# Kernel optimization log

Hardware: AMD Instinct MI355X
Metric: run time of the kernel (lower is better)

## Reference

```python
import jax, jax.numpy as jnp
import numpy as np

B, N, DIM = 2, 128, 128
H, DH = 8, 32
DI = H * DH          # dim_inner = 256
DM = 2 * DI          # mlp_expansion_factor * dim_inner = 512
MAXDEG = 2
S = 1 + MAXDEG + MAXDEG  # 5
M1, M2 = 3, 5        # 2l+1 for degrees 1,2


def setup_inputs() -> dict:
    key = jax.random.key(0)
    ks = jax.random.split(key, 24)
    rn = lambda k, shp, sc=1.0: jax.random.normal(k, shp, jnp.float32) * sc
    s_d = DIM ** -0.5
    s_m = DM ** -0.5
    s_i = DI ** -0.5
    return {
        "h":    rn(ks[0], (B, N, DIM)),
        "t_ij": rn(ks[1], (B, N, N, DIM)),
        "r1":   rn(ks[2], (B, N, N, M1)),
        "r2":   rn(ks[3], (B, N, N, M2)),
        "x1":   rn(ks[4], (B, N, DIM, M1)),
        "x2":   rn(ks[5], (B, N, DIM, M2)),
        # LayerNorm gains (bias=False)
        "g_hi": jnp.ones((DIM,), jnp.float32),
        "g_hj": jnp.ones((DIM,), jnp.float32),
        # projections (stored as [in, out])
        "Wq":  rn(ks[6],  (DIM, DI), s_d),
        "Wk":  rn(ks[7],  (DIM, DI), s_d),
        "Wv1": rn(ks[8],  (DIM, DM), s_d), "bv1": jnp.zeros((DM,), jnp.float32),
        "Wv2": rn(ks[9],  (DM, S * DI), s_m), "bv2": jnp.zeros((S * DI,), jnp.float32),
        "Wpv1": rn(ks[10], (DIM, DM), s_d), "bpv1": jnp.zeros((DM,), jnp.float32),
        "Wpv2": rn(ks[11], (DM, S * DI), s_m), "bpv2": jnp.zeros((S * DI,), jnp.float32),
        "Wek": rn(ks[12], (DIM, S * DI), s_d),
        "Wev": rn(ks[13], (DIM, S * DI), s_d),
        "Wg":  rn(ks[14], (DIM, H * S), s_d), "bg": jnp.zeros((H * S,), jnp.float32),
        "Wo":  rn(ks[15], (DI, DIM), s_i),
    }


def _ln(x, g):
    mu = x.mean(-1, keepdims=True)
    var = ((x - mu) ** 2).mean(-1, keepdims=True)
    return (x - mu) / jnp.sqrt(var + 1e-5) * g


def reference(h, t_ij, r1, r2, x1, x2, g_hi, g_hj, Wq, Wk, Wv1, bv1, Wv2, bv2,
              Wpv1, bpv1, Wpv2, bpv2, Wek, Wev, Wg, bg, Wo):
    silu = jax.nn.silu
    hi = _ln(h, g_hi)  # b n d
    hj = _ln(h, g_hj)
    # queries/keys: b h n dh
    q = (hi @ Wq).reshape(B, N, H, DH).transpose(0, 2, 1, 3)
    k = (hj @ Wk).reshape(B, N, H, DH).transpose(0, 2, 1, 3)
    # node values / post-attn values: b h n s dh
    v  = (silu(hj @ Wv1 + bv1) @ Wv2 + bv2).reshape(B, N, S, H, DH).transpose(0, 3, 1, 2, 4)
    pv = (silu(hj @ Wpv1 + bpv1) @ Wpv2 + bpv2).reshape(B, N, S, H, DH).transpose(0, 3, 1, 2, 4)
    # edge keys/values: b h i j s dh
    ek = silu(t_ij @ Wek).reshape(B, N, N, S, H, DH).transpose(0, 4, 1, 2, 3, 5)
    ev = (t_ij @ Wev).reshape(B, N, N, S, H, DH).transpose(0, 4, 1, 2, 3, 5)
    # keys elementwise-conditioned by edge keys, then score over dh
    sim = jnp.einsum('bhid,bhjd,bhijsd->bhijs', q, k, ek)
    attn = jax.nn.softmax(sim, axis=3)  # softmax over j (dim=-2 of b h i j s)
    # sea_ij: b h i j s dh
    sea = attn[..., None] * v[:, :, None] + ev * pv[:, :, None]
    # gates: b h i 1 s 1
    gates = jax.nn.sigmoid(hi @ Wg + bg).reshape(B, N, H, S).transpose(0, 2, 1, 3)
    out = sea * gates[:, :, :, None, :, None]
    # merge heads -> b i j s (h dh), combine -> b i j s dim
    out = out.transpose(0, 2, 3, 4, 1, 5).reshape(B, N, N, S, DI) @ Wo
    # split along s: (1, maxdeg, maxdeg) = (h_scales, r_scales, x_scales)
    h_out = h + out[..., 0, :].sum(axis=2)  # sum over j
    x1_out = (jnp.einsum('bjdm,bijd->bidm', x1, out[..., 3, :])
              + jnp.einsum('bijm,bijd->bidm', r1, out[..., 1, :]))
    x2_out = (jnp.einsum('bjdm,bijd->bidm', x2, out[..., 4, :])
              + jnp.einsum('bijm,bijd->bidm', r2, out[..., 2, :]))
    return (h_out, x1_out, x2_out)
```

## Files before the change

### kernel.cpp

```cpp
#include <hip/hip_runtime.h>
#include <math.h>

#define BB 2
#define NN 128
#define DD 128
#define DI 256
#define DM 512
#define SS 5
#define SDI 1280
#define HS 40
#define M1 3
#define M2 5

typedef __attribute__((ext_vector_type(8))) short bf16x8_t;
typedef __attribute__((ext_vector_type(4))) float f32x4_t;
typedef __attribute__((ext_vector_type(4))) float f32x4v;

#define MFMA __builtin_amdgcn_mfma_f32_16x16x32_bf16

__device__ __forceinline__ float sigm(float x){ return __fdividef(1.0f, 1.0f + __expf(-x)); }
__device__ __forceinline__ unsigned short f2bf(float f){
    union { float f; unsigned u; } v; v.f = f;
    unsigned r = v.u + 0x7FFFu + ((v.u>>16)&1u);
    return (unsigned short)(r>>16);
}
__device__ __forceinline__ unsigned pk2(float a, float b){
    return (unsigned)f2bf(a) | ((unsigned)f2bf(b)<<16);
}
__device__ __forceinline__ float bflo(unsigned u){ union{unsigned u; float f;} v; v.u = u<<16; return v.f; }
__device__ __forceinline__ float bfhi(unsigned u){ union{unsigned u; float f;} v; v.u = u & 0xFFFF0000u; return v.f; }

__global__ __launch_bounds__(256) void prep(
    const float* __restrict__ h,
    const float* __restrict__ g_hi, const float* __restrict__ g_hj,
    const float* __restrict__ Wq, const float* __restrict__ Wk,
    const float* __restrict__ Wv1, const float* __restrict__ Wpv1,
    const float* __restrict__ Wg,
    const float* __restrict__ Wek, const float* __restrict__ Wev,
    const float* __restrict__ Wo, const float* __restrict__ Wv2,
    const float* __restrict__ Wpv2,
    const float* __restrict__ x1, const float* __restrict__ x2,
    unsigned short* __restrict__ hi_ws, unsigned short* __restrict__ hj_ws,
    unsigned short* __restrict__ WekT, unsigned short* __restrict__ WevT,
    unsigned short* __restrict__ WoT, unsigned short* __restrict__ W2T,
    unsigned short* __restrict__ WnT,
    float* __restrict__ x1T, float* __restrict__ x2T)
{
    const int bx = blockIdx.x, tid = threadIdx.x;
    __shared__ unsigned short sLT[64*65];
    if (bx < 408){
        const float* src; unsigned short* dst; int W, ldD, R0, C0;
        int t = bx;
        if (t < 160){ src=Wv2;  dst=W2T;            W=SDI; ldD=DM;  R0=(t%20)*64; C0=(t/20)*64; }
        else if (t < 320){ t-=160; src=Wpv2; dst=W2T + SDI*DM; W=SDI; ldD=DM; R0=(t%20)*64; C0=(t/20)*64; }
        else if (t < 360){ t-=320; src=Wek; dst=WekT; W=SDI; ldD=DD; R0=(t%20)*64; C0=(t/20)*64; }
        else if (t < 400){ t-=360; src=Wev; dst=WevT; W=SDI; ldD=DD; R0=(t%20)*64; C0=(t/20)*64; }
        else { t-=400; src=Wo; dst=WoT; W=DD; ldD=DI; R0=(t%2)*64; C0=(t/2)*64; }
        const int tx = tid & 63, ty = tid >> 6;
        #pragma unroll
        for (int k=0;k<16;++k){
            int c = C0 + 4*k + ty;
            sLT[tx*65 + 4*k + ty] = f2bf(src[(size_t)c*W + R0 + tx]);
        }
        __syncthreads();
        #pragma unroll
        for (int k=0;k<16;++k){
            int rr = 4*k + ty;
            dst[(size_t)(R0+rr)*ldD + C0 + tx] = sLT[rr*65 + tx];
        }
    } else if (bx < 664){
        const int node = bx - 408;
        if (tid < 64){
            float h0 = h[node*DD + tid], h1 = h[node*DD + 64 + tid];
            float s1 = h0 + h1, s2 = h0*h0 + h1*h1;
            #pragma unroll
            for (int off=32; off; off>>=1){ s1 += __shfl_xor(s1,off); s2 += __shfl_xor(s2,off); }
            float mu   = s1*(1.0f/DD);
            float var  = s2*(1.0f/DD) - mu*mu;
            float rstd = rsqrtf(var + 1e-5f);
            float c0 = (h0-mu)*rstd, c1 = (h1-mu)*rstd;
            hi_ws[node*DD + tid]      = f2bf(c0*g_hi[tid]);
            hi_ws[node*DD + 64 + tid] = f2bf(c1*g_hi[64+tid]);
            hj_ws[node*DD + tid]      = f2bf(c0*g_hj[tid]);
            hj_ws[node*DD + 64 + tid] = f2bf(c1*g_hj[64+tid]);
        }
        for (int f = node*256 + tid; f < 1584*DD; f += 256*256){
            int row = f >> 7, d = f & 127;
            float v;
            if (row < 256)       v = Wq[d*DI + row];
            else if (row < 304){ int c = row-256; v = (c < HS) ? Wg[d*HS + c] : 0.0f; }
            else if (row < 560)  v = Wk[d*DI + (row-304)];
            else if (row < 1072) v = Wv1[d*DM + (row-560)];
            else                 v = Wpv1[d*DM + (row-1072)];
            WnT[f] = f2bf(v);
        }
    } else {
        const int t = bx - 664;
        const int bb = t >> 7, j = t & 127;
        const int d = tid & 127, half = tid >> 7;
        if (half == 0){
            #pragma unroll
            for (int m=0;m<M1;++m)
                x1T[((size_t)(bb*M1+m)*NN + j)*DD + d] =
                    x1[(((size_t)bb*NN + j)*DD + d)*M1 + m];
        } else {
            #pragma unroll
            for (int m=0;m<M2;++m)
                x2T[((size_t)(bb*M2+m)*NN + j)*DD + d] =
                    x2[(((size_t)bb*NN + j)*DD + d)*M2 + m];
        }
    }
}

__global__ __launch_bounds__(256,4) void node_gemm(
    const unsigned short* __restrict__ WnT,
    const unsigned short* __restrict__ hi_ws, const unsigned short* __restrict__ hj_ws,
    const float* __restrict__ bg, const float* __restrict__ bv1, const float* __restrict__ bpv1,
    float* __restrict__ q_ws, float* __restrict__ k_ws,
    float* __restrict__ g_ws, unsigned short* __restrict__ hid_ws)
{
    const int bx = blockIdx.x;
    const int tile = bx % 99, nq = bx / 99;
    const int tid = threadIdx.x, lane = tid&63, w = tid>>6;
    const int l15 = lane&15, g4 = lane>>4;
    const int ntile = nq*4 + w;
    const unsigned short* A  = WnT + (size_t)(tile*16 + l15)*DD + 8*g4;
    const unsigned short* Bp = ((tile < 19) ? hi_ws : hj_ws) + (size_t)(ntile*16 + l15)*DD + 8*g4;
    f32x4_t c = {0.f,0.f,0.f,0.f};
    #pragma unroll
    for (int ks=0; ks<4; ++ks)
        c = MFMA(*(const bf16x8_t*)(A + 32*ks), *(const bf16x8_t*)(Bp + 32*ks), c, 0,0,0);
    const int node = ntile*16 + l15;
    const int col0 = tile*16 + 4*g4;
    if (tile < 16){
        f32x4_t* dst = (f32x4_t*)(q_ws + (size_t)node*DI + col0);
        *dst = c;
    } else if (tile < 19){
        #pragma unroll
        for (int r=0;r<4;++r){
            int cc = col0 + r - 256;
            if (cc < HS) g_ws[node*HS + cc] = sigm(c[r] + bg[cc]);
        }
    } else if (tile < 35){
        f32x4_t* dst = (f32x4_t*)(k_ws + (size_t)node*DI + (col0-304));
        *dst = c;
    } else if (tile < 67){
        int cc = col0 - 560;
        float s0 = c[0]+bv1[cc], s1 = c[1]+bv1[cc+1], s2 = c[2]+bv1[cc+2], s3 = c[3]+bv1[cc+3];
        s0 *= sigm(s0); s1 *= sigm(s1); s2 *= sigm(s2); s3 *= sigm(s3);
        uint2 pkk; pkk.x = pk2(s0,s1); pkk.y = pk2(s2,s3);
        *(uint2*)(hid_ws + (size_t)node*1024 + cc) = pkk;
    } else {
        int cc = col0 - 1072;
        float s0 = c[0]+bpv1[cc], s1 = c[1]+bpv1[cc+1], s2 = c[2]+bpv1[cc+2], s3 = c[3]+bpv1[cc+3];
        s0 *= sigm(s0); s1 *= sigm(s1); s2 *= sigm(s2); s3 *= sigm(s3);
        uint2 pkk; pkk.x = pk2(s0,s1); pkk.y = pk2(s2,s3);
        *(uint2*)(hid_ws + (size_t)node*1024 + 512 + cc) = pkk;
    }
}

__global__ __launch_bounds__(256,4) void v2_gemm(
    const unsigned short* __restrict__ W2T,
    const unsigned short* __restrict__ hid_ws,
    const float* __restrict__ bv2, const float* __restrict__ bpv2,
    unsigned short* __restrict__ vpv_ws)
{
    const int bx = blockIdx.x;
    const int otile = bx % 160, nq = bx / 160;
    const int tid = threadIdx.x, lane = tid&63, w = tid>>6;
    const int l15 = lane&15, g4 = lane>>4;
    const int ntile = nq*4 + w;
    const int obase = otile*16;
    const int koff = (obase < SDI) ? 0 : 512;
    const unsigned short* A  = W2T + (size_t)(obase + l15)*DM + 8*g4;
    const unsigned short* Bp = hid_ws + (size_t)(ntile*16 + l15)*1024 + koff + 8*g4;
    f32x4_t c = {0.f,0.f,0.f,0.f};
    #pragma unroll
    for (int ks=0; ks<16; ++ks)
        c = MFMA(*(const bf16x8_t*)(A + 32*ks), *(const bf16x8_t*)(Bp + 32*ks), c, 0,0,0);
    const int node = ntile*16 + l15;
    const int o0 = obase + 4*g4;
    const float* bias = (obase < SDI) ? bv2 : bpv2;
    const int ob = (obase < SDI) ? o0 : (o0 - SDI);
    float v0 = c[0]+bias[ob], v1 = c[1]+bias[ob+1], v2 = c[2]+bias[ob+2], v3 = c[3]+bias[ob+3];
    uint2 pkk; pkk.x = pk2(v0,v1); pkk.y = pk2(v2,v3);
    *(uint2*)(vpv_ws + (size_t)node*2560 + o0) = pkk;
}

#define SH_T   0
#define SH_QK  16384
#define SH_SIM 49152
#define SH_Q   59392

__global__ __launch_bounds__(512,4) void simh(
    const float* __restrict__ t_ij,
    const unsigned short* __restrict__ WekT,
    const float* __restrict__ q_ws, const float* __restrict__ k_ws,
    float* __restrict__ sim_ws)
{
    __shared__ __align__(16) char sm[60416];
    float* sSIM = (float*)(sm + SH_SIM);
    float* sQf  = (float*)(sm + SH_Q);

    const int bx0 = blockIdx.x;
    const int bx = ((bx0 & 7) << 6) | (bx0 >> 3);
    const int node = bx >> 1, jh = bx & 1;
    const int b = node >> 7;
    const int j0 = jh*64;
    const int tid = threadIdx.x, lane = tid&63, w = tid>>6;
    const int l15 = lane&15, g4 = lane>>4;

    if (tid < DI) sQf[tid] = q_ws[(size_t)node*DI + tid];
    {
        const int j = tid>>3, seg = tid&7;
        const float* src = t_ij + (size_t)(node*NN + j0 + j)*DD + seg*16;
        char* row = sm + SH_T + j*256;
        const int swz = (j&7)<<4;
        #pragma unroll
        for (int u=0;u<4;++u){
            f32x4v tv = __builtin_nontemporal_load((const f32x4v*)(src + 4*u));
            uint2 pkk; pkk.x = pk2(tv[0],tv[1]); pkk.y = pk2(tv[2],tv[3]);
            *(uint2*)(row + ((2*(seg*16+4*u)) ^ swz)) = pkk;
        }
    }
    __syncthreads();
    {
        const int j = tid>>3, seg = tid&7;
        const float* kr = k_ws + (size_t)(b*NN + j0 + j)*DI + seg*32;
        char* row = sm + SH_QK + j*512;
        const int swz = (j&7)<<4;
        #pragma unroll
        for (int u=0;u<8;++u){
            float4 kv = *(const float4*)(kr + 4*u);
            const float* qv = sQf + seg*32 + 4*u;
            uint2 pkk; pkk.x = pk2(kv.x*qv[0], kv.y*qv[1]); pkk.y = pk2(kv.z*qv[2], kv.w*qv[3]);
            *(uint2*)(row + ((2*(seg*32+4*u)) ^ swz)) = pkk;
        }
    }
    bf16x8_t bT[4][4];
    #pragma unroll
    for (int jt=0;jt<4;++jt){
        const int jc = jt*16 + l15;
        const char* row = sm + SH_T + jc*256;
        const int swz = (jc&7)<<4;
        #pragma unroll
        for (int ks=0;ks<4;++ks)
            bT[jt][ks] = *(const bf16x8_t*)(row + ((2*(32*ks+8*g4)) ^ swz));
    }
    __syncthreads();

    for (int p5=0; p5<5; ++p5){
        const int p = w + 8*p5;
        const unsigned short* ap = WekT + (size_t)(2*p)*16*DD + (size_t)l15*DD + 8*g4;
        bf16x8_t a0[4], a1[4];
        #pragma unroll
        for (int ks=0;ks<4;++ks){
            a0[ks] = *(const bf16x8_t*)(ap + 32*ks);
            a1[ks] = *(const bf16x8_t*)(ap + 16*DD + 32*ks);
        }
        const int hs = w*SS + p5;
        const int o0 = 32*p + 4*g4;
        const int qk0 = o0 & 255;
        #pragma unroll
        for (int jt=0;jt<4;++jt){
            f32x4_t c0 = {0.f,0.f,0.f,0.f}, c1 = {0.f,0.f,0.f,0.f};
            #pragma unroll
            for (int ks=0;ks<4;++ks){
                c0 = MFMA(a0[ks], bT[jt][ks], c0, 0,0,0);
                c1 = MFMA(a1[ks], bT[jt][ks], c1, 0,0,0);
            }
            const int jr = jt*16 + l15;
            const char* qrow = sm + SH_QK + jr*512;
            const int swz = (jr&7)<<4;
            uint2 u0 = *(const uint2*)(qrow + ((2*qk0) ^ swz));
            uint2 u1 = *(const uint2*)(qrow + ((2*(qk0+16)) ^ swz));
            float part =
                (c0[0]*sigm(c0[0]))*bflo(u0.x) + (c0[1]*sigm(c0[1]))*bfhi(u0.x)
              + (c0[2]*sigm(c0[2]))*bflo(u0.y) + (c0[3]*sigm(c0[3]))*bfhi(u0.y)
              + (c1[0]*sigm(c1[0]))*bflo(u1.x) + (c1[1]*sigm(c1[1]))*bfhi(u1.x)
              + (c1[2]*sigm(c1[2]))*bflo(u1.y) + (c1[3]*sigm(c1[3]))*bfhi(u1.y);
            part += __shfl_xor(part, 16);
            part += __shfl_xor(part, 32);
            if (g4 == 0) sSIM[jr*HS + hs] = part;
        }
    }
    __syncthreads();
    {
        float* dst = sim_ws + (size_t)node*NN*HS + j0*HS;
        for (int t2=tid; t2<64*HS; t2+=512) dst[t2] = sSIM[t2];
    }
}

__global__ __launch_bounds__(256) void softmax_k(
    float* __restrict__ sim_ws, const float* __restrict__ g_ws)
{
    const int node = blockIdx.x;
    const int tid = threadIdx.x, lane = tid&63, w = tid>>6;
    float* srow = sim_ws + (size_t)node*NN*HS;
    #pragma unroll
    for (int u=0; u<10; ++u){
        const int hs = w*10 + u;
        const float gt = g_ws[node*HS + hs];
        float v0 = srow[lane*HS + hs];
        float v1 = srow[(lane+64)*HS + hs];
        float m = fmaxf(v0,v1);
        #pragma unroll
        for (int off=32; off; off>>=1) m = fmaxf(m, __shfl_xor(m,off));
        float e0 = __expf(v0-m), e1 = __expf(v1-m);
        float ssum = e0+e1;
        #pragma unroll
        for (int off=32; off; off>>=1) ssum += __shfl_xor(ssum,off);
        float inv = __fdividef(gt, ssum);
        srow[lane*HS + hs]      = e0*inv;
        srow[(lane+64)*HS + hs] = e1*inv;
    }
}

#define OH_T   0
#define OH_P   16384
#define OH_AT  49152
#define OH_G   59392
#define OH_W1  59552
#define OH_W2  60320

__global__ __launch_bounds__(512,4) void outh(
    const float* __restrict__ t_ij,
    const unsigned short* __restrict__ WevT, const unsigned short* __restrict__ WoT,
    const unsigned short* __restrict__ vpv_ws,
    const float* __restrict__ attn_ws,
    const float* __restrict__ g_ws,
    const float* __restrict__ r1, const float* __restrict__ r2,
    const float* __restrict__ x1T, const float* __restrict__ x2T,
    float* __restrict__ p_out)
{
    __shared__ __align__(16) char sm[61600];
    float* sATT = (float*)(sm + OH_AT);
    float* sG   = (float*)(sm + OH_G);
    float* sW1  = (float*)(sm + OH_W1);
    float* sW2  = (float*)(sm + OH_W2);

    const int bx0 = blockIdx.x;
    const int bx = ((bx0 & 7) << 6) | (bx0 >> 3);
    const int node = bx >> 1, jh = bx & 1;
    const int b = node >> 7;
    const int j0 = jh*64;
    const int tid = threadIdx.x, lane = tid&63, w = tid>>6;
    const int l15 = lane&15, g4 = lane>>4;

    {
        const int j = tid>>3, seg = tid&7;
        const float* src = t_ij + (size_t)(node*NN + j0 + j)*DD + seg*16;
        char* row = sm + OH_T + j*256;
        const int swz = (j&7)<<4;
        #pragma unroll
        for (int u=0;u<4;++u){
            f32x4v tv = __builtin_nontemporal_load((const f32x4v*)(src + 4*u));
            uint2 pkk; pkk.x = pk2(tv[0],tv[1]); pkk.y = pk2(tv[2],tv[3]);
            *(uint2*)(row + ((2*(seg*16+4*u)) ^ swz)) = pkk;
        }
    }
    {
        const float* asrc = attn_ws + (size_t)node*NN*HS + j0*HS;
        for (int t2=tid; t2<64*HS; t2+=512) sATT[t2] = asrc[t2];
    }
    if (tid < HS) sG[tid] = g_ws[node*HS + tid];
    if (tid < 64*M1) sW1[tid] = r1[((size_t)node*NN + j0)*M1 + tid];
    if (tid < 64*M2) sW2[tid] = r2[((size_t)node*NN + j0)*M2 + tid];
    bf16x8_t bWo[8];
    {
        const unsigned short* wr = WoT + (size_t)(w*16 + l15)*DI + 8*g4;
        #pragma unroll
        for (int ks=0;ks<8;++ks) bWo[ks] = *(const bf16x8_t*)(wr + 32*ks);
    }
    __syncthreads();

    const int d = w*16 + l15;
    float ah = 0.f;
    float ax1[M1] = {0.f,0.f,0.f};
    float ax2[M2] = {0.f,0.f,0.f,0.f,0.f};

    #pragma unroll
    for (int s=0; s<SS; ++s){
        #pragma unroll
        for (int mloc=0; mloc<2; ++mloc){
            const int mt = w*2 + mloc;
            const unsigned short* ap = WevT + (size_t)(s*DI + mt*16 + l15)*DD + 8*g4;
            bf16x8_t aa[4];
            #pragma unroll
            for (int ks=0;ks<4;++ks) aa[ks] = *(const bf16x8_t*)(ap + 32*ks);
            const int m0 = mt*16 + 4*g4;
            const int hh = mt >> 1;
            const float gtv = sG[hh*SS + s];
            #pragma unroll
            for (int jt=0;jt<4;++jt){
                const int jc = jt*16 + l15;
                bf16x8_t bT[4];
                {
                    const char* row = sm + OH_T + jc*256;
                    const int swz = (jc&7)<<4;
                    #pragma unroll
                    for (int ks=0;ks<4;++ks)
                        bT[ks] = *(const bf16x8_t*)(row + ((2*(32*ks+8*g4)) ^ swz));
                }
                f32x4_t c = {0.f,0.f,0.f,0.f};
                #pragma unroll
                for (int ks=0;ks<4;++ks) c = MFMA(aa[ks], bT[ks], c, 0,0,0);
                const float atv = sATT[jc*HS + hh*SS + s];
                const unsigned short* vb = vpv_ws + (size_t)(b*NN + j0 + jc)*2560 + s*DI + m0;
                uint2 vv = *(const uint2*)vb;
                uint2 pp = *(const uint2*)(vb + SDI);
                float q0 = atv*bflo(vv.x) + gtv*c[0]*bflo(pp.x);
                float q1 = atv*bfhi(vv.x) + gtv*c[1]*bfhi(pp.x);
                float q2 = atv*bflo(vv.y) + gtv*c[2]*bflo(pp.y);
                float q3 = atv*bfhi(vv.y) + gtv*c[3]*bfhi(pp.y);
                uint2 pkk; pkk.x = pk2(q0,q1); pkk.y = pk2(q2,q3);
                *(uint2*)(sm + OH_P + jc*512 + ((2*m0) ^ ((jc&7)<<4))) = pkk;
            }
        }
        __syncthreads();
        #pragma unroll
        for (int jt=0; jt<4; ++jt){
            const int arow = jt*16 + l15;
            const char* pb = sm + OH_P + arow*512;
            const int aswz = (arow&7)<<4;
            f32x4_t c = {0.f,0.f,0.f,0.f};
            #pragma unroll
            for (int ks=0;ks<8;++ks){
                bf16x8_t a = *(const bf16x8_t*)(pb + ((64*ks + 16*g4) ^ aswz));
                c = MFMA(a, bWo[ks], c, 0,0,0);
            }
            if (s == 0){
                ah += c[0]+c[1]+c[2]+c[3];
            } else if (s == 1){
                #pragma unroll
                for (int r=0;r<4;++r){
                    const int jr = jt*16 + 4*g4 + r;
                    #pragma unroll
                    for (int m=0;m<M1;++m) ax1[m] = fmaf(sW1[jr*M1+m], c[r], ax1[m]);
                }
            } else if (s == 2){
                #pragma unroll
                for (int r=0;r<4;++r){
                    const int jr = jt*16 + 4*g4 + r;
                    #pragma unroll
                    for (int m=0;m<M2;++m) ax2[m] = fmaf(sW2[jr*M2+m], c[r], ax2[m]);
                }
            } else if (s == 3){
                #pragma unroll
                for (int r=0;r<4;++r){
                    const int jr = j0 + jt*16 + 4*g4 + r;
                    #pragma unroll
                    for (int m=0;m<M1;++m)
                        ax1[m] = fmaf(x1T[((size_t)(b*M1+m)*NN + jr)*DD + d], c[r], ax1[m]);
                }
            } else {
                #pragma unroll
                for (int r=0;r<4;++r){
                    const int jr = j0 + jt*16 + 4*g4 + r;
                    #pragma unroll
                    for (int m=0;m<M2;++m)
                        ax2[m] = fmaf(x2T[((size_t)(b*M2+m)*NN + jr)*DD + d], c[r], ax2[m]);
                }
            }
        }
        __syncthreads();
    }

    {
        float v0 = ah;
        float v1 = ax1[0], v2 = ax1[1], v3 = ax1[2];
        float v4 = ax2[0], v5 = ax2[1], v6 = ax2[2], v7 = ax2[3], v8 = ax2[4];
        v0 += __shfl_xor(v0,16); v0 += __shfl_xor(v0,32);
        v1 += __shfl_xor(v1,16); v1 += __shfl_xor(v1,32);
        v2 += __shfl_xor(v2,16); v2 += __shfl_xor(v2,32);
        v3 += __shfl_xor(v3,16); v3 += __shfl_xor(v3,32);
        v4 += __shfl_xor(v4,16); v4 += __shfl_xor(v4,32);
        v5 += __shfl_xor(v5,16); v5 += __shfl_xor(v5,32);
        v6 += __shfl_xor(v6,16); v6 += __shfl_xor(v6,32);
        v7 += __shfl_xor(v7,16); v7 += __shfl_xor(v7,32);
        v8 += __shfl_xor(v8,16); v8 += __shfl_xor(v8,32);
        if (g4 == 0){
            float* pb = p_out + (size_t)bx*9*DD + d;
            pb[0*DD] = v0;
            pb[1*DD] = v1; pb[2*DD] = v2; pb[3*DD] = v3;
            pb[4*DD] = v4; pb[5*DD] = v5; pb[6*DD] = v6; pb[7*DD] = v7; pb[8*DD] = v8;
        }
    }
}

__global__ __launch_bounds__(128) void combine(
    const float* __restrict__ h, const float* __restrict__ p_out,
    float* __restrict__ out_h, float* __restrict__ out_x1, float* __restrict__ out_x2)
{
    const int node = blockIdx.x, d = threadIdx.x;
    const float* pa = p_out + (size_t)(node*2+0)*9*DD + d;
    const float* pb = p_out + (size_t)(node*2+1)*9*DD + d;
    out_h[(size_t)node*DD + d] = h[(size_t)node*DD + d] + pa[0] + pb[0];
    #pragma unroll
    for (int m=0;m<M1;++m)
        out_x1[((size_t)node*DD + d)*M1 + m] = pa[(1+m)*DD] + pb[(1+m)*DD];
    #pragma unroll
    for (int m=0;m<M2;++m)
        out_x2[((size_t)node*DD + d)*M2 + m] = pa[(4+m)*DD] + pb[(4+m)*DD];
}

extern "C" void kernel_launch(void* const* d_in, const int* in_sizes, int n_in,
                              void* d_out, int out_size, void* d_ws, size_t ws_size,
                              hipStream_t stream)
{
    (void)in_sizes; (void)n_in; (void)out_size; (void)ws_size;
    const float* h    = (const float*)d_in[0];
    const float* t_ij = (const float*)d_in[1];
    const float* r1   = (const float*)d_in[2];
    const float* r2   = (const float*)d_in[3];
    const float* x1   = (const float*)d_in[4];
    const float* x2   = (const float*)d_in[5];
    const float* g_hi = (const float*)d_in[6];
    const float* g_hj = (const float*)d_in[7];
    const float* Wq   = (const float*)d_in[8];
    const float* Wk   = (const float*)d_in[9];
    const float* Wv1  = (const float*)d_in[10];
    const float* bv1  = (const float*)d_in[11];
    const float* Wv2  = (const float*)d_in[12];
    const float* bv2  = (const float*)d_in[13];
    const float* Wpv1 = (const float*)d_in[14];
    const float* bpv1 = (const float*)d_in[15];
    const float* Wpv2 = (const float*)d_in[16];
    const float* bpv2 = (const float*)d_in[17];
    const float* Wek  = (const float*)d_in[18];
    const float* Wev  = (const float*)d_in[19];
    const float* Wg   = (const float*)d_in[20];
    const float* bg   = (const float*)d_in[21];
    const float* Wo   = (const float*)d_in[22];

    float* fb     = (float*)d_ws;
    float* q_ws   = fb;
    float* k_ws   = q_ws   + 65536;
    float* g_ws   = k_ws   + 65536;
    float* sim_ws = g_ws   + 10240;
    float* p_out  = sim_ws + 1310720;
    float* x1T    = p_out  + 589824;
    float* x2T    = x1T    + 98304;
    unsigned short* hi_ws  = (unsigned short*)(x2T + 163840);
    unsigned short* hj_ws  = hi_ws  + 32768;
    unsigned short* hid_ws = hj_ws  + 32768;
    unsigned short* vpv_ws = hid_ws + 262144;
    unsigned short* WekT   = vpv_ws + 655360;
    unsigned short* WevT   = WekT   + 163840;
    unsigned short* WoT    = WevT   + 163840;
    unsigned short* W2T    = WoT    + 32768;
    unsigned short* WnT    = W2T    + 1310720;

    float* out_h  = (float*)d_out;
    float* out_x1 = out_h  + BB*NN*DD;
    float* out_x2 = out_x1 + BB*NN*DD*M1;

    prep<<<920, 256, 0, stream>>>(h, g_hi, g_hj, Wq, Wk, Wv1, Wpv1, Wg,
        Wek, Wev, Wo, Wv2, Wpv2, x1, x2,
        hi_ws, hj_ws, WekT, WevT, WoT, W2T, WnT, x1T, x2T);

    node_gemm<<<396, 256, 0, stream>>>(WnT, hi_ws, hj_ws, bg, bv1, bpv1,
        q_ws, k_ws, g_ws, hid_ws);

    v2_gemm<<<640, 256, 0, stream>>>(W2T, hid_ws, bv2, bpv2, vpv_ws);

    simh<<<512, 512, 0, stream>>>(t_ij, WekT, q_ws, k_ws, sim_ws);

    softmax_k<<<256, 256, 0, stream>>>(sim_ws, g_ws);

    outh<<<512, 512, 0, stream>>>(t_ij, WevT, WoT, vpv_ws, sim_ws, g_ws,
        r1, r2, x1T, x2T, p_out);

    combine<<<256, 128, 0, stream>>>(h, p_out, out_h, out_x1, out_x2);
}
```

Baseline: 184.3 us.

## Reduce s=0..2 over j before the Wo projection and defer Wo to combine

For the scale channels whose j-weights do not depend on d (s=0,1,2), the outh kernel now sums the gated values over j in the DI space first, weighting by r1/r2. It writes these partial sums to a workspace, and the combine kernel applies the Wo projection to them afterwards. This drops three of the five per-tile Wo MFMA passes, along with their LDS staging and barriers. Only s=3 and s=4 still go through the P tile and Wo in outh, with the x loads issued ahead of the MFMAs. The cost is more cross-lane shuffle reductions, more register pressure for the accumulators, and a combine kernel that now does a small 9x256x128 matvec per node.

Result: faster. 172.5 us (-6.4%).

```diff
diff --git a/kernel.cpp b/kernel.cpp
--- a/kernel.cpp
+++ b/kernel.cpp
@@ -323,6 +323,80 @@
 #define OH_W1  59552
 #define OH_W2  60320
 
+#define EV_BODY(S, EPILOG)                                                        \
+    _Pragma("unroll")                                                             \
+    for (int mloc=0; mloc<2; ++mloc){                                             \
+        const int mt = w*2 + mloc;                                                \
+        const int m0 = mt*16 + 4*g4;                                              \
+        uint2 vvr[4], ppr[4];                                                     \
+        _Pragma("unroll")                                                         \
+        for (int jt=0;jt<4;++jt){                                                 \
+            const unsigned short* vb = vpv_ws + (size_t)(b*NN + j0 + jt*16 + l15)*2560 + (S)*DI + m0; \
+            vvr[jt] = *(const uint2*)vb;                                          \
+            ppr[jt] = *(const uint2*)(vb + SDI);                                  \
+        }                                                                         \
+        const unsigned short* ap = WevT + (size_t)((S)*DI + mt*16 + l15)*DD + 8*g4; \
+        bf16x8_t aa[4];                                                           \
+        _Pragma("unroll")                                                         \
+        for (int ks=0;ks<4;++ks) aa[ks] = *(const bf16x8_t*)(ap + 32*ks);         \
+        const int hh = mt >> 1;                                                   \
+        const float gtv = sG[hh*SS + (S)];                                        \
+        _Pragma("unroll")                                                         \
+        for (int jt=0;jt<4;++jt){                                                 \
+            const int jc = jt*16 + l15;                                           \
+            bf16x8_t bT[4];                                                       \
+            {   const char* row_ = sm + OH_T + jc*256;                            \
+                const int swz_ = (jc&7)<<4;                                       \
+                _Pragma("unroll")                                                 \
+                for (int ks=0;ks<4;++ks)                                          \
+                    bT[ks] = *(const bf16x8_t*)(row_ + ((2*(32*ks+8*g4)) ^ swz_)); } \
+            f32x4_t c = {0.f,0.f,0.f,0.f};                                        \
+            _Pragma("unroll")                                                     \
+            for (int ks=0;ks<4;++ks) c = MFMA(aa[ks], bT[ks], c, 0,0,0);          \
+            const float atv = sATT[jc*HS + hh*SS + (S)];                          \
+            float g_[4];                                                          \
+            g_[0] = atv*bflo(vvr[jt].x) + gtv*c[0]*bflo(ppr[jt].x);               \
+            g_[1] = atv*bfhi(vvr[jt].x) + gtv*c[1]*bfhi(ppr[jt].x);               \
+            g_[2] = atv*bflo(vvr[jt].y) + gtv*c[2]*bflo(ppr[jt].y);               \
+            g_[3] = atv*bfhi(vvr[jt].y) + gtv*c[3]*bfhi(ppr[jt].y);               \
+            EPILOG                                                                \
+        }                                                                         \
+    }
+
+#define WO_X(XT, MM, AX)                                                          \
+    _Pragma("unroll")                                                             \
+    for (int jt=0; jt<4; ++jt){                                                   \
+        float xv[4*(MM)];                                                         \
+        _Pragma("unroll")                                                         \
+        for (int r_=0;r_<4;++r_){                                                 \
+            const int jr = j0 + jt*16 + 4*g4 + r_;                                \
+            _Pragma("unroll")                                                     \
+            for (int m_=0;m_<(MM);++m_)                                           \
+                xv[r_*(MM)+m_] = XT[((size_t)(b*(MM)+m_)*NN + jr)*DD + d];        \
+        }                                                                         \
+        const int arow = jt*16 + l15;                                             \
+        const char* pbp = sm + OH_P + arow*512;                                   \
+        const int aswz = (arow&7)<<4;                                             \
+        f32x4_t c = {0.f,0.f,0.f,0.f};                                            \
+        _Pragma("unroll")                                                         \
+        for (int ks=0;ks<8;++ks){                                                 \
+            bf16x8_t a = *(const bf16x8_t*)(pbp + ((64*ks + 16*g4) ^ aswz));      \
+            c = MFMA(a, bWo[ks], c, 0,0,0);                                       \
+        }                                                                         \
+        _Pragma("unroll")                                                         \
+        for (int r_=0;r_<4;++r_){                                                 \
+            _Pragma("unroll")                                                     \
+            for (int m_=0;m_<(MM);++m_) AX[m_] = fmaf(xv[r_*(MM)+m_], c[r_], AX[m_]); \
+        }                                                                         \
+    }
+
+#define RED_WRITE(VAL, ROW, T_)                                                   \
+    { float v_ = (VAL);                                                           \
+      v_ += __shfl_xor(v_,1); v_ += __shfl_xor(v_,2);                             \
+      v_ += __shfl_xor(v_,4); v_ += __shfl_xor(v_,8);                             \
+      if (l15 == 0)                                                               \
+          pdst[(ROW)*256 + (w*2 + ((T_)>>2))*16 + 4*g4 + ((T_)&3)] = v_; }
+
 __global__ __launch_bounds__(512,4) void outh(
     const float* __restrict__ t_ij,
     const unsigned short* __restrict__ WevT, const unsigned short* __restrict__ WoT,
@@ -331,7 +405,7 @@
     const float* __restrict__ g_ws,
     const float* __restrict__ r1, const float* __restrict__ r2,
     const float* __restrict__ x1T, const float* __restrict__ x2T,
-    float* __restrict__ p_out)
+    float* __restrict__ p012, float* __restrict__ p34)
 {
     __shared__ __align__(16) char sm[61600];
     float* sATT = (float*)(sm + OH_AT);
@@ -366,110 +440,85 @@
     if (tid < HS) sG[tid] = g_ws[node*HS + tid];
     if (tid < 64*M1) sW1[tid] = r1[((size_t)node*NN + j0)*M1 + tid];
     if (tid < 64*M2) sW2[tid] = r2[((size_t)node*NN + j0)*M2 + tid];
+    __syncthreads();
+
+    float* pdst = p012 + (size_t)(jh*256 + node)*9*256;
+
+    {
+        float a0[8] = {0,0,0,0,0,0,0,0};
+        EV_BODY(0, {
+            _Pragma("unroll")
+            for (int k_=0;k_<4;++k_) a0[mloc*4+k_] += g_[k_];
+        })
+        #pragma unroll
+        for (int t_=0;t_<8;++t_) RED_WRITE(a0[t_], 0, t_)
+    }
+    {
+        float a1[M1][8];
+        #pragma unroll
+        for (int m_=0;m_<M1;++m_)
+            #pragma unroll
+            for (int t_=0;t_<8;++t_) a1[m_][t_] = 0.f;
+        EV_BODY(1, {
+            _Pragma("unroll")
+            for (int m_=0;m_<M1;++m_){
+                const float wgt = sW1[jc*M1 + m_];
+                _Pragma("unroll")
+                for (int k_=0;k_<4;++k_) a1[m_][mloc*4+k_] = fmaf(wgt, g_[k_], a1[m_][mloc*4+k_]);
+            }
+        })
+        #pragma unroll
+        for (int m_=0;m_<M1;++m_)
+            #pragma unroll
+            for (int t_=0;t_<8;++t_) RED_WRITE(a1[m_][t_], 1+m_, t_)
+    }
+    {
+        float a2[M2][8];
+        #pragma unroll
+        for (int m_=0;m_<M2;++m_)
+            #pragma unroll
+            for (int t_=0;t_<8;++t_) a2[m_][t_] = 0.f;
+        EV_BODY(2, {
+            _Pragma("unroll")
+            for (int m_=0;m_<M2;++m_){
+                const float wgt = sW2[jc*M2 + m_];
+                _Pragma("unroll")
+                for (int k_=0;k_<4;++k_) a2[m_][mloc*4+k_] = fmaf(wgt, g_[k_], a2[m_][mloc*4+k_]);
+            }
+        })
+        #pragma unroll
+        for (int m_=0;m_<M2;++m_)
+            #pragma unroll
+            for (int t_=0;t_<8;++t_) RED_WRITE(a2[m_][t_], 4+m_, t_)
+    }
+
+    const int d = w*16 + l15;
     bf16x8_t bWo[8];
     {
-        const unsigned short* wr = WoT + (size_t)(w*16 + l15)*DI + 8*g4;
+        const unsigned short* wr = WoT + (size_t)d*DI + 8*g4;
         #pragma unroll
         for (int ks=0;ks<8;++ks) bWo[ks] = *(const bf16x8_t*)(wr + 32*ks);
     }
-    __syncthreads();
-
-    const int d = w*16 + l15;
-    float ah = 0.f;
     float ax1[M1] = {0.f,0.f,0.f};
     float ax2[M2] = {0.f,0.f,0.f,0.f,0.f};
 
-    #pragma unroll
-    for (int s=0; s<SS; ++s){
-        #pragma unroll
-        for (int mloc=0; mloc<2; ++mloc){
-            const int mt = w*2 + mloc;
-            const unsigned short* ap = WevT + (size_t)(s*DI + mt*16 + l15)*DD + 8*g4;
-            bf16x8_t aa[4];
-            #pragma unroll
-            for (int ks=0;ks<4;++ks) aa[ks] = *(const bf16x8_t*)(ap + 32*ks);
-            const int m0 = mt*16 + 4*g4;
-            const int hh = mt >> 1;
-            const float gtv = sG[hh*SS + s];
-            #pragma unroll
-            for (int jt=0;jt<4;++jt){
-                const int jc = jt*16 + l15;
-                bf16x8_t bT[4];
-                {
-                    const char* row = sm + OH_T + jc*256;
-                    const int swz = (jc&7)<<4;
-                    #pragma unroll
-                    for (int ks=0;ks<4;++ks)
-                        bT[ks] = *(const bf16x8_t*)(row + ((2*(32*ks+8*g4)) ^ swz));
-                }
-                f32x4_t c = {0.f,0.f,0.f,0.f};
-                #pragma unroll
-                for (int ks=0;ks<4;++ks) c = MFMA(aa[ks], bT[ks], c, 0,0,0);
-                const float atv = sATT[jc*HS + hh*SS + s];
-                const unsigned short* vb = vpv_ws + (size_t)(b*NN + j0 + jc)*2560 + s*DI + m0;
-                uint2 vv = *(const uint2*)vb;
-                uint2 pp = *(const uint2*)(vb + SDI);
-                float q0 = atv*bflo(vv.x) + gtv*c[0]*bflo(pp.x);
-                float q1 = atv*bfhi(vv.x) + gtv*c[1]*bfhi(pp.x);
-                float q2 = atv*bflo(vv.y) + gtv*c[2]*bflo(pp.y);
-                float q3 = atv*bfhi(vv.y) + gtv*c[3]*bfhi(pp.y);
-                uint2 pkk; pkk.x = pk2(q0,q1); pkk.y = pk2(q2,q3);
-                *(uint2*)(sm + OH_P + jc*512 + ((2*m0) ^ ((jc&7)<<4))) = pkk;
-            }
-        }
-        __syncthreads();
-        #pragma unroll
-        for (int jt=0; jt<4; ++jt){
-            const int arow = jt*16 + l15;
-            const char* pb = sm + OH_P + arow*512;
-            const int aswz = (arow&7)<<4;
-            f32x4_t c = {0.f,0.f,0.f,0.f};
-            #pragma unroll
-            for (int ks=0;ks<8;++ks){
-                bf16x8_t a = *(const bf16x8_t*)(pb + ((64*ks + 16*g4) ^ aswz));
-                c = MFMA(a, bWo[ks], c, 0,0,0);
-            }
-            if (s == 0){
-                ah += c[0]+c[1]+c[2]+c[3];
-            } else if (s == 1){
-                #pragma unroll
-                for (int r=0;r<4;++r){
-                    const int jr = jt*16 + 4*g4 + r;
-                    #pragma unroll
-                    for (int m=0;m<M1;++m) ax1[m] = fmaf(sW1[jr*M1+m], c[r], ax1[m]);
-                }
-            } else if (s == 2){
-                #pragma unroll
-                for (int r=0;r<4;++r){
-                    const int jr = jt*16 + 4*g4 + r;
-                    #pragma unroll
-                    for (int m=0;m<M2;++m) ax2[m] = fmaf(sW2[jr*M2+m], c[r], ax2[m]);
-                }
-            } else if (s == 3){
-                #pragma unroll
-                for (int r=0;r<4;++r){
-                    const int jr = j0 + jt*16 + 4*g4 + r;
-                    #pragma unroll
-                    for (int m=0;m<M1;++m)
-                        ax1[m] = fmaf(x1T[((size_t)(b*M1+m)*NN + jr)*DD + d], c[r], ax1[m]);
-                }
-            } else {
-                #pragma unroll
-                for (int r=0;r<4;++r){
-                    const int jr = j0 + jt*16 + 4*g4 + r;
-                    #pragma unroll
-                    for (int m=0;m<M2;++m)
-                        ax2[m] = fmaf(x2T[((size_t)(b*M2+m)*NN + jr)*DD + d], c[r], ax2[m]);
-                }
-            }
-        }
-        __syncthreads();
-    }
-
-    {
-        float v0 = ah;
-        float v1 = ax1[0], v2 = ax1[1], v3 = ax1[2];
-        float v4 = ax2[0], v5 = ax2[1], v6 = ax2[2], v7 = ax2[3], v8 = ax2[4];
+    EV_BODY(3, {
+        uint2 pkk; pkk.x = pk2(g_[0],g_[1]); pkk.y = pk2(g_[2],g_[3]);
+        *(uint2*)(sm + OH_P + jc*512 + ((2*m0) ^ ((jc&7)<<4))) = pkk;
+    })
+    __syncthreads();
+    WO_X(x1T, M1, ax1)
+    __syncthreads();
+    EV_BODY(4, {
+        uint2 pkk; pkk.x = pk2(g_[0],g_[1]); pkk.y = pk2(g_[2],g_[3]);
+        *(uint2*)(sm + OH_P + jc*512 + ((2*m0) ^ ((jc&7)<<4))) = pkk;
+    })
+    __syncthreads();
+    WO_X(x2T, M2, ax2)
+
+    {
+        float v0 = ax1[0], v1 = ax1[1], v2 = ax1[2];
+        float v3 = ax2[0], v4 = ax2[1], v5 = ax2[2], v6 = ax2[3], v7 = ax2[4];
         v0 += __shfl_xor(v0,16); v0 += __shfl_xor(v0,32);
         v1 += __shfl_xor(v1,16); v1 += __shfl_xor(v1,32);
         v2 += __shfl_xor(v2,16); v2 += __shfl_xor(v2,32);
@@ -478,30 +527,66 @@
         v5 += __shfl_xor(v5,16); v5 += __shfl_xor(v5,32);
         v6 += __shfl_xor(v6,16); v6 += __shfl_xor(v6,32);
         v7 += __shfl_xor(v7,16); v7 += __shfl_xor(v7,32);
-        v8 += __shfl_xor(v8,16); v8 += __shfl_xor(v8,32);
         if (g4 == 0){
-            float* pb = p_out + (size_t)bx*9*DD + d;
-            pb[0*DD] = v0;
-            pb[1*DD] = v1; pb[2*DD] = v2; pb[3*DD] = v3;
-            pb[4*DD] = v4; pb[5*DD] = v5; pb[6*DD] = v6; pb[7*DD] = v7; pb[8*DD] = v8;
+            float* pb = p34 + (size_t)bx*8*DD + d;
+            pb[0*DD] = v0; pb[1*DD] = v1; pb[2*DD] = v2;
+            pb[3*DD] = v3; pb[4*DD] = v4; pb[5*DD] = v5;
+            pb[6*DD] = v6; pb[7*DD] = v7;
         }
     }
 }
 
 __global__ __launch_bounds__(128) void combine(
-    const float* __restrict__ h, const float* __restrict__ p_out,
+    const float* __restrict__ h, const unsigned short* __restrict__ WoT,
+    const float* __restrict__ p012, const float* __restrict__ p34,
     float* __restrict__ out_h, float* __restrict__ out_x1, float* __restrict__ out_x2)
 {
+    __shared__ float sZ[256*12];
     const int node = blockIdx.x, d = threadIdx.x;
-    const float* pa = p_out + (size_t)(node*2+0)*9*DD + d;
-    const float* pb = p_out + (size_t)(node*2+1)*9*DD + d;
-    out_h[(size_t)node*DD + d] = h[(size_t)node*DD + d] + pa[0] + pb[0];
+    const float* pa = p012 + ((size_t)node*9)*256;
+    const float* pb = p012 + ((size_t)(256 + node)*9)*256;
+    for (int t=d; t<2304; t+=128){
+        int m = t >> 8, c = t & 255;
+        sZ[c*12 + m] = pa[t] + pb[t];
+    }
+    __syncthreads();
+    float az[9] = {0.f,0.f,0.f,0.f,0.f,0.f,0.f,0.f,0.f};
+    const unsigned short* wr = WoT + (size_t)d*DI;
+    for (int cb=0; cb<32; ++cb){
+        uint4 wv = *(const uint4*)(wr + cb*8);
+        float wk[8];
+        wk[0]=bflo(wv.x); wk[1]=bfhi(wv.x); wk[2]=bflo(wv.y); wk[3]=bfhi(wv.y);
+        wk[4]=bflo(wv.z); wk[5]=bfhi(wv.z); wk[6]=bflo(wv.w); wk[7]=bfhi(wv.w);
+        #pragma unroll
+        for (int k=0;k<8;++k){
+            const float* zb = sZ + (cb*8+k)*12;
+            float4 za = *(const float4*)zb;
+            float4 zbv = *(const float4*)(zb+4);
+            float z8 = zb[8];
+            az[0] = fmaf(za.x,  wk[k], az[0]);
+            az[1] = fmaf(za.y,  wk[k], az[1]);
+            az[2] = fmaf(za.z,  wk[k], az[2]);
+            az[3] = fmaf(za.w,  wk[k], az[3]);
+            az[4] = fmaf(zbv.x, wk[k], az[4]);
+            az[5] = fmaf(zbv.y, wk[k], az[5]);
+            az[6] = fmaf(zbv.z, wk[k], az[6]);
+            az[7] = fmaf(zbv.w, wk[k], az[7]);
+            az[8] = fmaf(z8,    wk[k], az[8]);
+        }
+    }
+    float p34v[8];
+    #pragma unroll
+    for (int row=0; row<8; ++row){
+        p34v[row] = p34[((size_t)(node*2+0)*8 + row)*DD + d]
+                  + p34[((size_t)(node*2+1)*8 + row)*DD + d];
+    }
+    out_h[(size_t)node*DD + d] = h[(size_t)node*DD + d] + az[0];
     #pragma unroll
     for (int m=0;m<M1;++m)
-        out_x1[((size_t)node*DD + d)*M1 + m] = pa[(1+m)*DD] + pb[(1+m)*DD];
+        out_x1[((size_t)node*DD + d)*M1 + m] = az[1+m] + p34v[m];
     #pragma unroll
     for (int m=0;m<M2;++m)
-        out_x2[((size_t)node*DD + d)*M2 + m] = pa[(4+m)*DD] + pb[(4+m)*DD];
+        out_x2[((size_t)node*DD + d)*M2 + m] = az[4+m] + p34v[3+m];
 }
 
 extern "C" void kernel_launch(void* const* d_in, const int* in_sizes, int n_in,
@@ -538,8 +623,9 @@
     float* k_ws   = q_ws   + 65536;
     float* g_ws   = k_ws   + 65536;
     float* sim_ws = g_ws   + 10240;
-    float* p_out  = sim_ws + 1310720;
-    float* x1T    = p_out  + 589824;
+    float* p012   = sim_ws + 1310720;
+    float* p34    = p012   + 1179648;
+    float* x1T    = p34    + 524288;
     float* x2T    = x1T    + 98304;
     unsigned short* hi_ws  = (unsigned short*)(x2T + 163840);
     unsigned short* hj_ws  = hi_ws  + 32768;
@@ -569,7 +655,7 @@
     softmax_k<<<256, 256, 0, stream>>>(sim_ws, g_ws);
 
     outh<<<512, 512, 0, stream>>>(t_ij, WevT, WoT, vpv_ws, sim_ws, g_ws,
-        r1, r2, x1T, x2T, p_out);
-
-    combine<<<256, 128, 0, stream>>>(h, p_out, out_h, out_x1, out_x2);
-}
+        r1, r2, x1T, x2T, p012, p34);
+
+    combine<<<256, 128, 0, stream>>>(h, WoT, p012, p34, out_h, out_x1, out_x2);
+}
```
